# Kernel tuning notes

Measured on AMD Instinct MI355X. Metric: run time of the kernel, lower is better.

## Reference

```python
import jax, jax.numpy as jnp
import numpy as np

N = 100000
E = 1600000
IN_C, HID_C, OUT_C = 128, 128, 64


def setup_inputs() -> dict:
    key = jax.random.key(0)
    ks = jax.random.split(key, 8)
    x = jax.random.normal(ks[0], (N, IN_C), dtype=jnp.float32)
    edge_index = jax.random.randint(ks[1], (2, E), 0, N, dtype=jnp.int64)
    # GCNConv weights (lin has no bias; bias added after aggregation)
    s1 = 1.0 / np.sqrt(IN_C)
    s2 = 1.0 / np.sqrt(HID_C)
    W1 = jax.random.uniform(ks[2], (IN_C, HID_C), jnp.float32, -s1, s1)
    b1 = jnp.zeros((HID_C,), jnp.float32)
    W2 = jax.random.uniform(ks[3], (HID_C, HID_C), jnp.float32, -s2, s2)
    b2 = jnp.zeros((HID_C,), jnp.float32)
    W3 = jax.random.uniform(ks[4], (HID_C, OUT_C), jnp.float32, -s2, s2)
    b3 = jnp.zeros((OUT_C,), jnp.float32)
    return {"x": x, "edge_index": edge_index, "W1": W1, "b1": b1,
            "W2": W2, "b2": b2, "W3": W3, "b3": b3}


def _prep_graph(edge_index):
    # add self-loops, compute symmetric normalization D^-1/2 A D^-1/2
    loop = jnp.arange(N, dtype=edge_index.dtype)
    src = jnp.concatenate([edge_index[0], loop])
    dst = jnp.concatenate([edge_index[1], loop])
    deg = jax.ops.segment_sum(jnp.ones_like(dst, dtype=jnp.float32), dst, num_segments=N)
    dinv = jnp.where(deg > 0, jax.lax.rsqrt(jnp.maximum(deg, 1e-12)), 0.0)
    norm = dinv[src] * dinv[dst]  # [E+N]
    return src, dst, norm


def _gcn_conv(x, W, b, src, dst, norm):
    h = x @ W                               # [N, C_out]
    msg = h[src] * norm[:, None]            # gather + scale, [E+N, C_out]
    out = jax.ops.segment_sum(msg, dst, num_segments=N)  # scatter-add
    return out + b


def reference(x, edge_index, W1, b1, W2, b2, W3, b3):
    src, dst, norm = _prep_graph(edge_index)
    h = jax.nn.relu(_gcn_conv(x, W1, b1, src, dst, norm))
    h = jax.nn.relu(_gcn_conv(h, W2, b2, src, dst, norm))
    return _gcn_conv(h, W3, b3, src, dst, norm)
```

## Files before the change

### kernel.cpp

```cpp
#include <hip/hip_runtime.h>
#include <hip/hip_bf16.h>
#include <hip/hip_fp16.h>

#define NN 100000
#define NE 1600000
constexpr int NN_PAD = 100032;
constexpr int NBUK = (NN + 255) / 256;
constexpr int CH   = 4096;
constexpr int EPT  = CH / 256;
constexpr int NCHK = (NE + CH - 1) / CH;
constexpr int LCNT = NBUK * NCHK;
constexpr int SCB  = (LCNT + 1023) / 1024;

typedef _Float16 f16x8 __attribute__((ext_vector_type(8)));
typedef float f32x4 __attribute__((ext_vector_type(4)));

__device__ __forceinline__ float h2f(unsigned short h) {
    return __half2float(__ushort_as_half(h));
}
__device__ __forceinline__ unsigned short f2h(float f) {
    return __half_as_ushort(__float2half(f));
}

__global__ void k_detect_i64(const unsigned* __restrict__ ei, int* __restrict__ flag) {
    __shared__ int any_nz;
    if (threadIdx.x == 0) any_nz = 0;
    __syncthreads();
    int nz = 0;
    for (int i = threadIdx.x; i < 2048; i += 256)
        if (ei[2 * i + 1] != 0u) nz = 1;
    if (nz) atomicExch(&any_nz, 1);
    __syncthreads();
    if (threadIdx.x == 0) *flag = (any_nz == 0) ? 1 : 0;
}

__device__ __forceinline__ int edge_at(const void* ei, int is64, long long idx) {
    if (is64) return (int)((const long long*)ei)[idx];
    return ((const int*)ei)[idx];
}

__global__ __launch_bounds__(256) void k_count(const void* __restrict__ ei,
                                               const int* __restrict__ flag,
                                               int* __restrict__ counts) {
    __shared__ int cnt[NBUK];
    const int t = threadIdx.x, blk = blockIdx.x;
    for (int i = t; i < NBUK; i += 256) cnt[i] = 0;
    __syncthreads();
    const int is64 = *flag;
    const int e0 = blk * CH;
    const int elim = min(NE, e0 + CH);
#pragma unroll
    for (int j = 0; j < EPT; j++) {
        int e = e0 + j * 256 + t;
        if (e < elim) {
            int s = edge_at(ei, is64, e);
            int d = edge_at(ei, is64, (long long)NE + e);
            if ((unsigned)s < NN && (unsigned)d < NN) atomicAdd(&cnt[d >> 8], 1);
        }
    }
    __syncthreads();
    for (int i = t; i < NBUK; i += 256) counts[(size_t)i * NCHK + blk] = cnt[i];
}

__global__ void k_scan1v(int* __restrict__ data, int* __restrict__ bsum) {
    __shared__ int lds[256];
    int t = threadIdx.x, b = blockIdx.x;
    int base = b * 1024 + t * 4;
    int v0 = (base + 0 < LCNT) ? data[base + 0] : 0;
    int v1 = (base + 1 < LCNT) ? data[base + 1] : 0;
    int v2 = (base + 2 < LCNT) ? data[base + 2] : 0;
    int v3 = (base + 3 < LCNT) ? data[base + 3] : 0;
    lds[t] = v0 + v1 + v2 + v3;
    __syncthreads();
    for (int off = 1; off < 256; off <<= 1) {
        int x = (t >= off) ? lds[t - off] : 0;
        __syncthreads();
        lds[t] += x;
        __syncthreads();
    }
    int excl = (t > 0) ? lds[t - 1] : 0;
    if (t == 255) bsum[b] = lds[255];
    if (base + 0 < LCNT) data[base + 0] = excl;
    if (base + 1 < LCNT) data[base + 1] = excl + v0;
    if (base + 2 < LCNT) data[base + 2] = excl + v0 + v1;
    if (base + 3 < LCNT) data[base + 3] = excl + v0 + v1 + v2;
}

__global__ void k_scan2v(int* __restrict__ bsum) {
    __shared__ int lds[256];
    int t = threadIdx.x;
    int v = (t < SCB) ? bsum[t] : 0;
    lds[t] = v;
    __syncthreads();
    for (int off = 1; off < 256; off <<= 1) {
        int x = (t >= off) ? lds[t - off] : 0;
        __syncthreads();
        lds[t] += x;
        __syncthreads();
    }
    if (t < SCB) bsum[t] = lds[t] - v;
    if (t == SCB - 1) bsum[SCB] = lds[t];
}

__global__ void k_scan3v(int* __restrict__ data, const int* __restrict__ bsum) {
    int i = blockIdx.x * 256 + threadIdx.x;
    if (i < LCNT) data[i] += bsum[i >> 10];
    else if (i == LCNT) data[LCNT] = bsum[SCB];
}

__global__ __launch_bounds__(256) void k_scatter2(const void* __restrict__ ei,
                                                  const int* __restrict__ flag,
                                                  const int* __restrict__ scanned,
                                                  unsigned* __restrict__ staging) {
    __shared__ int cnt[512], excl[512], cur[512], gbase[512];
    __shared__ unsigned lbuf[CH];
    __shared__ unsigned short lbkt[CH];
    const int t = threadIdx.x, blk = blockIdx.x;
    cnt[t] = 0; cnt[t + 256] = 0;
    __syncthreads();
    const int is64 = *flag;
    const int e0 = blk * CH;
    const int elim = min(NE, e0 + CH);
    unsigned recs[EPT];
    int bkts[EPT];
#pragma unroll
    for (int j = 0; j < EPT; j++) {
        int e = e0 + j * 256 + t;
        int bk = -1; unsigned rc = 0;
        if (e < elim) {
            int s = edge_at(ei, is64, e);
            int d = edge_at(ei, is64, (long long)NE + e);
            if ((unsigned)s < NN && (unsigned)d < NN) {
                bk = d >> 8;
                rc = (unsigned)s | ((unsigned)(d & 255) << 17);
                atomicAdd(&cnt[bk], 1);
            }
        }
        recs[j] = rc; bkts[j] = bk;
    }
    __syncthreads();
    excl[t] = cnt[t]; excl[t + 256] = cnt[t + 256];
    __syncthreads();
    for (int off = 1; off < 512; off <<= 1) {
        int a0 = (t >= off) ? excl[t - off] : 0;
        int a1 = (t + 256 >= off) ? excl[t + 256 - off] : 0;
        __syncthreads();
        excl[t] += a0; excl[t + 256] += a1;
        __syncthreads();
    }
    int i0 = excl[t] - cnt[t], i1 = excl[t + 256] - cnt[t + 256];
    excl[t] = i0; excl[t + 256] = i1;
    cur[t] = i0; cur[t + 256] = i1;
    for (int b = t; b < NBUK; b += 256) gbase[b] = scanned[(size_t)b * NCHK + blk];
    __syncthreads();
#pragma unroll
    for (int j = 0; j < EPT; j++) {
        if (bkts[j] >= 0) {
            int pos = atomicAdd(&cur[bkts[j]], 1);
            lbuf[pos] = recs[j];
            lbkt[pos] = (unsigned short)bkts[j];
        }
    }
    __syncthreads();
    const int tot = excl[NBUK];
    for (int i = t; i < tot; i += 256) {
        int b = lbkt[i];
        staging[(size_t)gbase[b] + (i - excl[b])] = lbuf[i];
    }
}

__global__ __launch_bounds__(256) void k_phaseB2(const unsigned* __restrict__ staging,
                                                 const int* __restrict__ scanned,
                                                 float* __restrict__ dinv,
                                                 int* __restrict__ row_off,
                                                 int* __restrict__ csr) {
    __shared__ int cnt[256], excl[256], cur[256];
    __shared__ int buf[8192];
    const int t = threadIdx.x, b = blockIdx.x;
    const int node0 = b << 8;
    const int nlocal = min(256, NN - node0);
    const int seg_beg = scanned[(size_t)b * NCHK];
    const size_t nxt = (size_t)(b + 1) * NCHK;
    const int seg_end = scanned[nxt > (size_t)LCNT ? (size_t)LCNT : nxt];
    const int len = min(seg_end - seg_beg, 8192);
    cnt[t] = 0;
    __syncthreads();
    for (int i = t; i < len; i += 256) {
        unsigned r = staging[seg_beg + i];
        atomicAdd(&cnt[r >> 17], 1);
    }
    __syncthreads();
    excl[t] = cnt[t];
    __syncthreads();
    for (int off = 1; off < 256; off <<= 1) {
        int x = (t >= off) ? excl[t - off] : 0;
        __syncthreads();
        excl[t] += x;
        __syncthreads();
    }
    int ex = excl[t] - cnt[t];
    excl[t] = ex;
    cur[t] = ex;
    if (t < nlocal) {
        row_off[node0 + t] = seg_beg + ex;
        dinv[node0 + t] = rsqrtf((float)(cnt[t] + 1));
    }
    if (b == NBUK - 1 && t == 0) row_off[NN] = seg_end;
    __syncthreads();
    for (int i = t; i < len; i += 256) {
        unsigned r = staging[seg_beg + i];
        int pos = atomicAdd(&cur[r >> 17], 1);
        buf[pos] = (int)(r & 0x1FFFFu);
    }
    __syncthreads();
    for (int i = t; i < len; i += 256) csr[seg_beg + i] = buf[i];
}

template <int C>
__global__ void k_packW(const float* __restrict__ W, _Float16* __restrict__ P) {
    constexpr int NT = C / 16;
    int i = blockIdx.x * 256 + threadIdx.x;
    if (i >= 4 * NT * 512) return;
    int j = i & 7, lane = (i >> 3) & 63;
    int rest = i >> 9;
    int ct = rest % NT, kc = rest / NT;
    int k = kc * 32 + (lane >> 4) * 8 + j;
    int n = ct * 16 + (lane & 15);
    P[i] = (_Float16)W[k * C + n];
}

template <int C, bool F32SRC>
__global__ __launch_bounds__(256) void k_mgemm(const void* __restrict__ Xv,
                                               const _Float16* __restrict__ P,
                                               const float* __restrict__ dinv,
                                               unsigned short* __restrict__ H) {
    constexpr int NT = C / 16;
    const int tid = threadIdx.x, w = tid >> 6, lane = tid & 63;
    const int lr = lane & 15, lg = lane >> 4;
    const int row = blockIdx.x * 64 + w * 16 + lr;
    const int arow = F32SRC ? min(row, NN - 1) : row;
    f32x4 acc[NT];
#pragma unroll
    for (int t = 0; t < NT; t++) acc[t] = (f32x4){0.f, 0.f, 0.f, 0.f};
    const f16x8* __restrict__ Pp = (const f16x8*)P;
#pragma unroll
    for (int kc = 0; kc < 4; kc++) {
        f16x8 a;
        if (F32SRC) {
            const float* xp = (const float*)Xv + (size_t)arow * 128 + kc * 32 + lg * 8;
            float4 x0 = *(const float4*)xp;
            float4 x1 = *(const float4*)(xp + 4);
            a[0] = (_Float16)x0.x; a[1] = (_Float16)x0.y;
            a[2] = (_Float16)x0.z; a[3] = (_Float16)x0.w;
            a[4] = (_Float16)x1.x; a[5] = (_Float16)x1.y;
            a[6] = (_Float16)x1.z; a[7] = (_Float16)x1.w;
        } else {
            a = *(const f16x8*)((const _Float16*)Xv + (size_t)arow * 128 + kc * 32 + lg * 8);
        }
#pragma unroll
        for (int t = 0; t < NT; t++) {
            f16x8 b = Pp[(kc * NT + t) * 64 + lane];
            acc[t] = __builtin_amdgcn_mfma_f32_16x16x32_f16(a, b, acc[t], 0, 0, 0);
        }
    }
    const int orow0 = blockIdx.x * 64 + w * 16 + lg * 4;
    float dv[4];
#pragma unroll
    for (int r = 0; r < 4; r++) dv[r] = dinv[orow0 + r];
#pragma unroll
    for (int t = 0; t < NT; t++)
#pragma unroll
        for (int r = 0; r < 4; r++)
            H[(size_t)(orow0 + r) * C + t * 16 + lr] = f2h(acc[t][r] * dv[r]);
}

template <bool RELU>
__global__ __launch_bounds__(256) void k_agg128(const unsigned short* __restrict__ H,
                                                const int* __restrict__ row_off,
                                                const int* __restrict__ csr,
                                                const float* __restrict__ dinv,
                                                const float* __restrict__ bias,
                                                unsigned short* __restrict__ OUT) {
    const int tid = threadIdx.x;
    const int wid = tid >> 6, lane = tid & 63;
    const int half = lane >> 5, il = lane & 31;
    const int node = blockIdx.x * 8 + wid * 2 + half;
    const int beg = row_off[node];
    const int cnt = row_off[node + 1] - beg;
    const int tmax = max(cnt, __shfl(cnt, lane ^ 32));
    const ushort4* __restrict__ Hh = (const ushort4*)H;
    float4 acc = make_float4(0.f, 0.f, 0.f, 0.f);
    for (int j0 = 0; j0 < tmax; j0 += 32) {
        int sidx = node;
        if (j0 + il < cnt) sidx = csr[beg + j0 + il];
        const int rem = min(32, tmax - j0);
        for (int u = 0; u < rem; u += 8) {
            ushort4 v[8]; float m[8];
#pragma unroll
            for (int k = 0; k < 8; k++) {
                int s = __shfl(sidx, half * 32 + u + k);
                v[k] = Hh[(size_t)s * 32 + il];
                m[k] = (j0 + u + k < cnt) ? 1.f : 0.f;
            }
#pragma unroll
            for (int k = 0; k < 8; k++) {
                acc.x = fmaf(m[k], h2f(v[k].x), acc.x);
                acc.y = fmaf(m[k], h2f(v[k].y), acc.y);
                acc.z = fmaf(m[k], h2f(v[k].z), acc.z);
                acc.w = fmaf(m[k], h2f(v[k].w), acc.w);
            }
        }
    }
    ushort4 hv = Hh[(size_t)node * 32 + il];
    acc.x += h2f(hv.x); acc.y += h2f(hv.y);
    acc.z += h2f(hv.z); acc.w += h2f(hv.w);
    const float dv = dinv[node];
    float4 bb = ((const float4*)bias)[il];
    float ox = fmaf(acc.x, dv, bb.x), oy = fmaf(acc.y, dv, bb.y);
    float oz = fmaf(acc.z, dv, bb.z), ow = fmaf(acc.w, dv, bb.w);
    if (RELU) {
        ox = fmaxf(ox, 0.f); oy = fmaxf(oy, 0.f);
        oz = fmaxf(oz, 0.f); ow = fmaxf(ow, 0.f);
    }
    ushort4 oh;
    oh.x = f2h(ox); oh.y = f2h(oy); oh.z = f2h(oz); oh.w = f2h(ow);
    ((ushort4*)OUT)[(size_t)node * 32 + il] = oh;
}

__global__ __launch_bounds__(256) void k_agg64(const unsigned short* __restrict__ H,
                                               const int* __restrict__ row_off,
                                               const int* __restrict__ csr,
                                               const float* __restrict__ dinv,
                                               const float* __restrict__ bias,
                                               float* __restrict__ OUT) {
    const int tid = threadIdx.x;
    const int wid = tid >> 6, lane = tid & 63;
    const int q = lane >> 4, il = lane & 15;
    const int node = blockIdx.x * 16 + wid * 4 + q;
    const int beg = row_off[node];
    const int cnt = row_off[node + 1] - beg;
    int m1 = max(cnt, __shfl(cnt, lane ^ 16));
    const int tmax = max(m1, __shfl(m1, lane ^ 32));
    const ushort4* __restrict__ Hh = (const ushort4*)H;
    float4 acc = make_float4(0.f, 0.f, 0.f, 0.f);
    for (int j0 = 0; j0 < tmax; j0 += 16) {
        int sidx = node;
        if (j0 + il < cnt) sidx = csr[beg + j0 + il];
        const int rem = min(16, tmax - j0);
        for (int u = 0; u < rem; u += 8) {
            ushort4 v[8]; float m[8];
#pragma unroll
            for (int k = 0; k < 8; k++) {
                int s = __shfl(sidx, q * 16 + u + k);
                v[k] = Hh[(size_t)s * 16 + il];
                m[k] = (j0 + u + k < cnt) ? 1.f : 0.f;
            }
#pragma unroll
            for (int k = 0; k < 8; k++) {
                acc.x = fmaf(m[k], h2f(v[k].x), acc.x);
                acc.y = fmaf(m[k], h2f(v[k].y), acc.y);
                acc.z = fmaf(m[k], h2f(v[k].z), acc.z);
                acc.w = fmaf(m[k], h2f(v[k].w), acc.w);
            }
        }
    }
    ushort4 hv = Hh[(size_t)node * 16 + il];
    acc.x += h2f(hv.x); acc.y += h2f(hv.y);
    acc.z += h2f(hv.z); acc.w += h2f(hv.w);
    const float dv = dinv[node];
    float4 bb = ((const float4*)bias)[il];
    float4 o;
    o.x = fmaf(acc.x, dv, bb.x); o.y = fmaf(acc.y, dv, bb.y);
    o.z = fmaf(acc.z, dv, bb.z); o.w = fmaf(acc.w, dv, bb.w);
    ((float4*)OUT)[(size_t)node * 16 + il] = o;
}

extern "C" void kernel_launch(void* const* d_in, const int* in_sizes, int n_in,
                              void* d_out, int out_size, void* d_ws, size_t ws_size,
                              hipStream_t stream) {
    const float* x  = (const float*)d_in[0];
    const void*  ei = d_in[1];
    const float* W1 = (const float*)d_in[2];
    const float* b1 = (const float*)d_in[3];
    const float* W2 = (const float*)d_in[4];
    const float* b2 = (const float*)d_in[5];
    const float* W3 = (const float*)d_in[6];
    const float* b3 = (const float*)d_in[7];
    float* out = (float*)d_out;

    char* wsp = (char*)d_ws;
    size_t off = 0;
    auto alloc = [&](size_t bytes) -> void* {
        void* p = wsp + off;
        off += (bytes + 255) & ~(size_t)255;
        return p;
    };
    unsigned short* G = (unsigned short*)alloc((size_t)NN_PAD * 128 * 2);
    unsigned short* F = (unsigned short*)alloc((size_t)NN_PAD * 128 * 2);
    float* dinv    = (float*)alloc((size_t)NN_PAD * 4);
    int*   row_off = (int*)alloc(((size_t)NN + 1) * 4);
    int*   counts  = (int*)alloc(((size_t)LCNT + 1) * 4);
    int*   bsum    = (int*)alloc(((size_t)SCB + 1) * 4);
    int*   csr     = (int*)alloc((size_t)NE * 4);
    _Float16* P1   = (_Float16*)alloc((size_t)128 * 128 * 2);
    _Float16* P2   = (_Float16*)alloc((size_t)128 * 128 * 2);
    _Float16* P3   = (_Float16*)alloc((size_t)128 * 64 * 2);
    int*   flag    = (int*)alloc(256);
    if (off > ws_size) return;

    unsigned* staging = (unsigned*)G;

    k_detect_i64<<<1, 256, 0, stream>>>((const unsigned*)ei, flag);
    k_count<<<NCHK, 256, 0, stream>>>(ei, flag, counts);
    k_scan1v<<<SCB, 256, 0, stream>>>(counts, bsum);
    k_scan2v<<<1, 256, 0, stream>>>(bsum);
    k_scan3v<<<(LCNT + 1 + 255) / 256, 256, 0, stream>>>(counts, bsum);
    k_scatter2<<<NCHK, 256, 0, stream>>>(ei, flag, counts, staging);
    k_phaseB2<<<NBUK, 256, 0, stream>>>(staging, counts, dinv, row_off, csr);

    k_packW<128><<<64, 256, 0, stream>>>(W1, P1);
    k_packW<128><<<64, 256, 0, stream>>>(W2, P2);
    k_packW<64><<<32, 256, 0, stream>>>(W3, P3);

    constexpr int NBLK = NN_PAD / 64;
    k_mgemm<128, true><<<NBLK, 256, 0, stream>>>(x, P1, dinv, G);
    k_agg128<true><<<NN / 8, 256, 0, stream>>>(G, row_off, csr, dinv, b1, F);
    k_mgemm<128, false><<<NBLK, 256, 0, stream>>>(F, P2, dinv, G);
    k_agg128<true><<<NN / 8, 256, 0, stream>>>(G, row_off, csr, dinv, b2, F);
    k_mgemm<64, false><<<NBLK, 256, 0, stream>>>(F, P3, dinv, G);
    k_agg64<<<NN / 16, 256, 0, stream>>>(G, row_off, csr, dinv, b3, out);
}
```

Before: 246.0 us.

## Fold graph-prep launches, halve edge chunk, widen agg64 loads

Removes the separate int64-detection and scan-finalize kernels by detecting per block and adding block sums on the fly, and merges three weight-pack launches into one. Halves the edge chunk size for counting/scatter, changing grid size and LDS use. Reworks the final 64-channel aggregation to use 8-lane groups with 16-byte loads per node. Adds redundant per-block detection reads and extra bsum lookups.

```diff
diff --git a/kernel.cpp b/kernel.cpp
--- a/kernel.cpp
+++ b/kernel.cpp
@@ -6,32 +6,21 @@
 #define NE 1600000
 constexpr int NN_PAD = 100032;
 constexpr int NBUK = (NN + 255) / 256;
-constexpr int CH   = 4096;
+constexpr int CH   = 2048;
 constexpr int EPT  = CH / 256;
 constexpr int NCHK = (NE + CH - 1) / CH;
 constexpr int LCNT = NBUK * NCHK;
-constexpr int SCB  = (LCNT + 1023) / 1024;
+constexpr int SCB  = (LCNT + 2047) / 2048;
 
 typedef _Float16 f16x8 __attribute__((ext_vector_type(8)));
 typedef float f32x4 __attribute__((ext_vector_type(4)));
+typedef unsigned short u16x8 __attribute__((ext_vector_type(8)));
 
 __device__ __forceinline__ float h2f(unsigned short h) {
     return __half2float(__ushort_as_half(h));
 }
 __device__ __forceinline__ unsigned short f2h(float f) {
     return __half_as_ushort(__float2half(f));
-}
-
-__global__ void k_detect_i64(const unsigned* __restrict__ ei, int* __restrict__ flag) {
-    __shared__ int any_nz;
-    if (threadIdx.x == 0) any_nz = 0;
-    __syncthreads();
-    int nz = 0;
-    for (int i = threadIdx.x; i < 2048; i += 256)
-        if (ei[2 * i + 1] != 0u) nz = 1;
-    if (nz) atomicExch(&any_nz, 1);
-    __syncthreads();
-    if (threadIdx.x == 0) *flag = (any_nz == 0) ? 1 : 0;
 }
 
 __device__ __forceinline__ int edge_at(const void* ei, int is64, long long idx) {
@@ -39,14 +28,25 @@
     return ((const int*)ei)[idx];
 }
 
+__device__ __forceinline__ int detect_is64_block(const void* ei, int* s_nz) {
+    const unsigned* e32 = (const unsigned*)ei;
+    int nz = 0;
+    for (int i = threadIdx.x; i < 512; i += 256)
+        if (e32[2 * i + 1] != 0u) nz = 1;
+    if (nz) *s_nz = 1;
+    __syncthreads();
+    return (*s_nz == 0) ? 1 : 0;
+}
+
 __global__ __launch_bounds__(256) void k_count(const void* __restrict__ ei,
-                                               const int* __restrict__ flag,
                                                int* __restrict__ counts) {
     __shared__ int cnt[NBUK];
+    __shared__ int s_nz;
     const int t = threadIdx.x, blk = blockIdx.x;
     for (int i = t; i < NBUK; i += 256) cnt[i] = 0;
-    __syncthreads();
-    const int is64 = *flag;
+    if (t == 0) s_nz = 0;
+    __syncthreads();
+    const int is64 = detect_is64_block(ei, &s_nz);
     const int e0 = blk * CH;
     const int elim = min(NE, e0 + CH);
 #pragma unroll
@@ -65,12 +65,14 @@
 __global__ void k_scan1v(int* __restrict__ data, int* __restrict__ bsum) {
     __shared__ int lds[256];
     int t = threadIdx.x, b = blockIdx.x;
-    int base = b * 1024 + t * 4;
-    int v0 = (base + 0 < LCNT) ? data[base + 0] : 0;
-    int v1 = (base + 1 < LCNT) ? data[base + 1] : 0;
-    int v2 = (base + 2 < LCNT) ? data[base + 2] : 0;
-    int v3 = (base + 3 < LCNT) ? data[base + 3] : 0;
-    lds[t] = v0 + v1 + v2 + v3;
+    int base = b * 2048 + t * 8;
+    int v[8], s = 0;
+#pragma unroll
+    for (int j = 0; j < 8; j++) {
+        v[j] = (base + j < LCNT) ? data[base + j] : 0;
+        s += v[j];
+    }
+    lds[t] = s;
     __syncthreads();
     for (int off = 1; off < 256; off <<= 1) {
         int x = (t >= off) ? lds[t - off] : 0;
@@ -78,12 +80,13 @@
         lds[t] += x;
         __syncthreads();
     }
-    int excl = (t > 0) ? lds[t - 1] : 0;
+    int run = (t > 0) ? lds[t - 1] : 0;
     if (t == 255) bsum[b] = lds[255];
-    if (base + 0 < LCNT) data[base + 0] = excl;
-    if (base + 1 < LCNT) data[base + 1] = excl + v0;
-    if (base + 2 < LCNT) data[base + 2] = excl + v0 + v1;
-    if (base + 3 < LCNT) data[base + 3] = excl + v0 + v1 + v2;
+#pragma unroll
+    for (int j = 0; j < 8; j++) {
+        if (base + j < LCNT) data[base + j] = run;
+        run += v[j];
+    }
 }
 
 __global__ void k_scan2v(int* __restrict__ bsum) {
@@ -102,23 +105,19 @@
     if (t == SCB - 1) bsum[SCB] = lds[t];
 }
 
-__global__ void k_scan3v(int* __restrict__ data, const int* __restrict__ bsum) {
-    int i = blockIdx.x * 256 + threadIdx.x;
-    if (i < LCNT) data[i] += bsum[i >> 10];
-    else if (i == LCNT) data[LCNT] = bsum[SCB];
-}
-
 __global__ __launch_bounds__(256) void k_scatter2(const void* __restrict__ ei,
-                                                  const int* __restrict__ flag,
-                                                  const int* __restrict__ scanned,
+                                                  const int* __restrict__ counts,
+                                                  const int* __restrict__ bsum,
                                                   unsigned* __restrict__ staging) {
     __shared__ int cnt[512], excl[512], cur[512], gbase[512];
     __shared__ unsigned lbuf[CH];
     __shared__ unsigned short lbkt[CH];
+    __shared__ int s_nz;
     const int t = threadIdx.x, blk = blockIdx.x;
     cnt[t] = 0; cnt[t + 256] = 0;
-    __syncthreads();
-    const int is64 = *flag;
+    if (t == 0) s_nz = 0;
+    __syncthreads();
+    const int is64 = detect_is64_block(ei, &s_nz);
     const int e0 = blk * CH;
     const int elim = min(NE, e0 + CH);
     unsigned recs[EPT];
@@ -151,7 +150,10 @@
     int i0 = excl[t] - cnt[t], i1 = excl[t + 256] - cnt[t + 256];
     excl[t] = i0; excl[t + 256] = i1;
     cur[t] = i0; cur[t + 256] = i1;
-    for (int b = t; b < NBUK; b += 256) gbase[b] = scanned[(size_t)b * NCHK + blk];
+    for (int bb = t; bb < NBUK; bb += 256) {
+        int idx = bb * NCHK + blk;
+        gbase[bb] = counts[idx] + bsum[idx >> 11];
+    }
     __syncthreads();
 #pragma unroll
     for (int j = 0; j < EPT; j++) {
@@ -170,7 +172,8 @@
 }
 
 __global__ __launch_bounds__(256) void k_phaseB2(const unsigned* __restrict__ staging,
-                                                 const int* __restrict__ scanned,
+                                                 const int* __restrict__ counts,
+                                                 const int* __restrict__ bsum,
                                                  float* __restrict__ dinv,
                                                  int* __restrict__ row_off,
                                                  int* __restrict__ csr) {
@@ -179,11 +182,18 @@
     const int t = threadIdx.x, b = blockIdx.x;
     const int node0 = b << 8;
     const int nlocal = min(256, NN - node0);
-    const int seg_beg = scanned[(size_t)b * NCHK];
-    const size_t nxt = (size_t)(b + 1) * NCHK;
-    const int seg_end = scanned[nxt > (size_t)LCNT ? (size_t)LCNT : nxt];
+    const int i0 = b * NCHK;
+    const int seg_beg = counts[i0] + bsum[i0 >> 11];
+    int seg_end;
+    if (b == NBUK - 1) {
+        seg_end = bsum[SCB];
+    } else {
+        const int i1 = (b + 1) * NCHK;
+        seg_end = counts[i1] + bsum[i1 >> 11];
+    }
     const int len = min(seg_end - seg_beg, 8192);
     cnt[t] = 0;
+    if (b == 0 && t < NN_PAD - NN) dinv[NN + t] = 0.f;
     __syncthreads();
     for (int i = t; i < len; i += 256) {
         unsigned r = staging[seg_beg + i];
@@ -217,16 +227,24 @@
 }
 
 template <int C>
-__global__ void k_packW(const float* __restrict__ W, _Float16* __restrict__ P) {
+__device__ __forceinline__ void packone(const float* __restrict__ W,
+                                        _Float16* __restrict__ P, int i) {
     constexpr int NT = C / 16;
-    int i = blockIdx.x * 256 + threadIdx.x;
-    if (i >= 4 * NT * 512) return;
     int j = i & 7, lane = (i >> 3) & 63;
     int rest = i >> 9;
     int ct = rest % NT, kc = rest / NT;
     int k = kc * 32 + (lane >> 4) * 8 + j;
     int n = ct * 16 + (lane & 15);
     P[i] = (_Float16)W[k * C + n];
+}
+
+__global__ void k_pack(const float* __restrict__ W1, const float* __restrict__ W2,
+                       const float* __restrict__ W3, _Float16* __restrict__ P1,
+                       _Float16* __restrict__ P2, _Float16* __restrict__ P3) {
+    int i = blockIdx.x * 256 + threadIdx.x;
+    if (i < 16384) packone<128>(W1, P1, i);
+    else if (i < 32768) packone<128>(W2, P2, i - 16384);
+    else if (i < 40960) packone<64>(W3, P3, i - 32768);
 }
 
 template <int C, bool F32SRC>
@@ -335,44 +353,45 @@
                                                float* __restrict__ OUT) {
     const int tid = threadIdx.x;
     const int wid = tid >> 6, lane = tid & 63;
-    const int q = lane >> 4, il = lane & 15;
-    const int node = blockIdx.x * 16 + wid * 4 + q;
+    const int q = lane >> 3, il = lane & 7;
+    const int node = blockIdx.x * 32 + wid * 8 + q;
     const int beg = row_off[node];
     const int cnt = row_off[node + 1] - beg;
-    int m1 = max(cnt, __shfl(cnt, lane ^ 16));
+    int m1 = max(cnt, __shfl(cnt, lane ^ 8));
+    m1 = max(m1, __shfl(m1, lane ^ 16));
     const int tmax = max(m1, __shfl(m1, lane ^ 32));
-    const ushort4* __restrict__ Hh = (const ushort4*)H;
-    float4 acc = make_float4(0.f, 0.f, 0.f, 0.f);
-    for (int j0 = 0; j0 < tmax; j0 += 16) {
+    const u16x8* __restrict__ Hh = (const u16x8*)H;
+    float acc[8] = {0.f, 0.f, 0.f, 0.f, 0.f, 0.f, 0.f, 0.f};
+    for (int j0 = 0; j0 < tmax; j0 += 8) {
         int sidx = node;
         if (j0 + il < cnt) sidx = csr[beg + j0 + il];
-        const int rem = min(16, tmax - j0);
-        for (int u = 0; u < rem; u += 8) {
-            ushort4 v[8]; float m[8];
-#pragma unroll
-            for (int k = 0; k < 8; k++) {
-                int s = __shfl(sidx, q * 16 + u + k);
-                v[k] = Hh[(size_t)s * 16 + il];
-                m[k] = (j0 + u + k < cnt) ? 1.f : 0.f;
-            }
-#pragma unroll
-            for (int k = 0; k < 8; k++) {
-                acc.x = fmaf(m[k], h2f(v[k].x), acc.x);
-                acc.y = fmaf(m[k], h2f(v[k].y), acc.y);
-                acc.z = fmaf(m[k], h2f(v[k].z), acc.z);
-                acc.w = fmaf(m[k], h2f(v[k].w), acc.w);
-            }
-        }
-    }
-    ushort4 hv = Hh[(size_t)node * 16 + il];
-    acc.x += h2f(hv.x); acc.y += h2f(hv.y);
-    acc.z += h2f(hv.z); acc.w += h2f(hv.w);
+        u16x8 v[8]; float m[8];
+#pragma unroll
+        for (int k = 0; k < 8; k++) {
+            int s = __shfl(sidx, q * 8 + k);
+            v[k] = Hh[(size_t)s * 8 + il];
+            m[k] = (j0 + k < cnt) ? 1.f : 0.f;
+        }
+#pragma unroll
+        for (int k = 0; k < 8; k++)
+#pragma unroll
+            for (int e = 0; e < 8; e++)
+                acc[e] = fmaf(m[k], h2f(v[k][e]), acc[e]);
+    }
+    u16x8 hv = Hh[(size_t)node * 8 + il];
+#pragma unroll
+    for (int e = 0; e < 8; e++) acc[e] += h2f(hv[e]);
     const float dv = dinv[node];
-    float4 bb = ((const float4*)bias)[il];
-    float4 o;
-    o.x = fmaf(acc.x, dv, bb.x); o.y = fmaf(acc.y, dv, bb.y);
-    o.z = fmaf(acc.z, dv, bb.z); o.w = fmaf(acc.w, dv, bb.w);
-    ((float4*)OUT)[(size_t)node * 16 + il] = o;
+    float4 b0 = *(const float4*)&bias[il * 8];
+    float4 b1 = *(const float4*)&bias[il * 8 + 4];
+    float ob[8] = {b0.x, b0.y, b0.z, b0.w, b1.x, b1.y, b1.z, b1.w};
+    float4 o0, o1;
+    o0.x = fmaf(acc[0], dv, ob[0]); o0.y = fmaf(acc[1], dv, ob[1]);
+    o0.z = fmaf(acc[2], dv, ob[2]); o0.w = fmaf(acc[3], dv, ob[3]);
+    o1.x = fmaf(acc[4], dv, ob[4]); o1.y = fmaf(acc[5], dv, ob[5]);
+    o1.z = fmaf(acc[6], dv, ob[6]); o1.w = fmaf(acc[7], dv, ob[7]);
+    *(float4*)&OUT[(size_t)node * 64 + il * 8] = o0;
+    *(float4*)&OUT[(size_t)node * 64 + il * 8 + 4] = o1;
 }
 
 extern "C" void kernel_launch(void* const* d_in, const int* in_sizes, int n_in,
@@ -405,22 +424,16 @@
     _Float16* P1   = (_Float16*)alloc((size_t)128 * 128 * 2);
     _Float16* P2   = (_Float16*)alloc((size_t)128 * 128 * 2);
     _Float16* P3   = (_Float16*)alloc((size_t)128 * 64 * 2);
-    int*   flag    = (int*)alloc(256);
     if (off > ws_size) return;
 
     unsigned* staging = (unsigned*)G;
 
-    k_detect_i64<<<1, 256, 0, stream>>>((const unsigned*)ei, flag);
-    k_count<<<NCHK, 256, 0, stream>>>(ei, flag, counts);
+    k_count<<<NCHK, 256, 0, stream>>>(ei, counts);
     k_scan1v<<<SCB, 256, 0, stream>>>(counts, bsum);
     k_scan2v<<<1, 256, 0, stream>>>(bsum);
-    k_scan3v<<<(LCNT + 1 + 255) / 256, 256, 0, stream>>>(counts, bsum);
-    k_scatter2<<<NCHK, 256, 0, stream>>>(ei, flag, counts, staging);
-    k_phaseB2<<<NBUK, 256, 0, stream>>>(staging, counts, dinv, row_off, csr);
-
-    k_packW<128><<<64, 256, 0, stream>>>(W1, P1);
-    k_packW<128><<<64, 256, 0, stream>>>(W2, P2);
-    k_packW<64><<<32, 256, 0, stream>>>(W3, P3);
+    k_scatter2<<<NCHK, 256, 0, stream>>>(ei, counts, bsum, staging);
+    k_phaseB2<<<NBUK, 256, 0, stream>>>(staging, counts, bsum, dinv, row_off, csr);
+    k_pack<<<160, 256, 0, stream>>>(W1, W2, W3, P1, P2, P3);
 
     constexpr int NBLK = NN_PAD / 64;
     k_mgemm<128, true><<<NBLK, 256, 0, stream>>>(x, P1, dinv, G);
@@ -428,5 +441,5 @@
     k_mgemm<128, false><<<NBLK, 256, 0, stream>>>(F, P2, dinv, G);
     k_agg128<true><<<NN / 8, 256, 0, stream>>>(G, row_off, csr, dinv, b2, F);
     k_mgemm<64, false><<<NBLK, 256, 0, stream>>>(F, P3, dinv, G);
-    k_agg64<<<NN / 16, 256, 0, stream>>>(G, row_off, csr, dinv, b3, out);
-}
+    k_agg64<<<NN / 32, 256, 0, stream>>>(G, row_off, csr, dinv, b3, out);
+}
```

Result: faster. 236.8 us, median of 2 (-3.8%).
